# Kernel tuning notes

Measured on AMD Instinct MI355X. Metric: run time of the kernel, lower is better.

## Reference

```python
import math
import jax, jax.numpy as jnp
import numpy as np

B, S, H, I, E = 4, 2048, 1024, 4096, 8
CAPACITY_FACTOR = 1.0


def setup_inputs() -> dict:
    key = jax.random.key(0)
    k1, k2, k3, k4, k5 = jax.random.split(key, 5)
    x = jax.random.normal(k1, (B, S, H), dtype=jnp.float32)
    # Router: nn.Linear(H, E) with xavier_uniform weight, zero-ish bias
    limit = math.sqrt(6.0 / (H + E))
    router_w = jax.random.uniform(k2, (E, H), dtype=jnp.float32, minval=-limit, maxval=limit)
    router_b = jnp.zeros((E,), dtype=jnp.float32)
    # Expert weights (torch.randn init; scaled for numeric sanity)
    experts_inter = jax.random.normal(k3, (E, H, I), dtype=jnp.float32) * 0.02
    experts_out = jax.random.normal(k4, (E, I, H), dtype=jnp.float32) * 0.02
    return {"x": x, "router_w": router_w, "router_b": router_b,
            "experts_inter": experts_inter, "experts_out": experts_out}


def reference(x, router_w, router_b, experts_inter, experts_out):
    b, s, h = x.shape
    e = experts_inter.shape[0]
    capacity = math.ceil(b * s / e * CAPACITY_FACTOR)  # static

    # Router: linear + softmax over experts
    routing_weights = jax.nn.softmax(x @ router_w.T + router_b, axis=-1)  # [b,s,e]

    x_flat = x.reshape(-1, h)                       # [N, h]
    w_flat = routing_weights.reshape(-1, e)         # [N, e]

    # softmax > 0 everywhere, but keep faithful mask-based routing
    routing_mask = (w_flat > 0).astype(jnp.int32)   # [N, e]
    # stable descending sort per expert column (matches stable torch.sort)
    sorted_indices = jnp.argsort(-routing_mask, axis=0, stable=True)  # [N, e]
    sorted_mask = jnp.take_along_axis(routing_mask, sorted_indices, axis=0)[:capacity]  # [c, e]
    sorted_indices = sorted_indices[:capacity]      # [c, e]

    used_tokens_indices = (sorted_indices * sorted_mask).reshape(-1)  # [c*e]
    mask_f = sorted_mask.reshape(-1).astype(x.dtype)[:, None]
    inputs_tokens = x_flat[used_tokens_indices] * mask_f              # [c*e, h]
    inputs_tokens = inputs_tokens.reshape(capacity, e, h)             # [c, e, h]
    inputs_weights = jnp.take_along_axis(w_flat, sorted_indices, axis=0)  # [c, e]

    # grouped expert FFN
    inter = jnp.einsum('ceh,ehi->cei', inputs_tokens, experts_inter)  # [c, e, I]
    inter = jax.nn.relu(inter)
    out = jnp.einsum('cei,eih->ceh', inter, experts_out)              # [c, e, h]
    out = out * inputs_weights[..., None]
    out = out.reshape(-1, h)                                          # [c*e, h]

    # scatter-add combine
    combined = jnp.zeros_like(x_flat).at[used_tokens_indices].add(out)
    return combined.reshape(b, s, h)
```

## Files before the change

### kernel.cpp

```cpp
#include <hip/hip_runtime.h>
#include <stdint.h>

#define H_DIM 1024
#define I_DIM 4096
#define E_NUM 8
#define CAP   1024

typedef __attribute__((ext_vector_type(8))) short bf16x8;
typedef __attribute__((ext_vector_type(4))) float f32x4;

#define AS1 __attribute__((address_space(1)))
#define AS3 __attribute__((address_space(3)))

__device__ __forceinline__ unsigned short f2bf(float f){
  union { float f; uint32_t u; } v; v.f = f;
  uint32_t u = v.u;
  uint32_t r = (u + 0x7FFFu + ((u >> 16) & 1u)) >> 16;
  return (unsigned short)r;
}

__global__ void zero_kernel(float4* __restrict__ p, int n4){
  int i = blockIdx.x*blockDim.x + threadIdx.x;
  int stride = gridDim.x*blockDim.x;
  float4 z; z.x=0.f; z.y=0.f; z.z=0.f; z.w=0.f;
  for (; i < n4; i += stride) p[i] = z;
}

__global__ __launch_bounds__(256) void router_kernel(
    const float* __restrict__ x, const float* __restrict__ rw_w,
    const float* __restrict__ rb, unsigned short* __restrict__ xb,
    float* __restrict__ rwout)
{
  int c = blockIdx.x;
  int t = threadIdx.x;
  float acc[E_NUM];
  #pragma unroll
  for (int e=0;e<E_NUM;e++) acc[e]=0.f;
  const float* xr = x + (size_t)c*H_DIM;
  for (int h=t; h<H_DIM; h+=256){
    float xv = xr[h];
    xb[(size_t)c*H_DIM + h] = f2bf(xv);
    #pragma unroll
    for (int e=0;e<E_NUM;e++) acc[e] += xv * rw_w[e*H_DIM + h];
  }
  __shared__ float part[256][E_NUM];
  #pragma unroll
  for (int e=0;e<E_NUM;e++) part[t][e]=acc[e];
  __syncthreads();
  for (int s=128; s>0; s>>=1){
    if (t<s){
      #pragma unroll
      for (int e=0;e<E_NUM;e++) part[t][e]+=part[t+s][e];
    }
    __syncthreads();
  }
  if (t==0){
    float l[E_NUM], mx=-1e30f;
    #pragma unroll
    for (int e=0;e<E_NUM;e++){ l[e]=part[0][e]+rb[e]; mx=fmaxf(mx,l[e]); }
    float s=0.f;
    #pragma unroll
    for (int e=0;e<E_NUM;e++){ l[e]=expf(l[e]-mx); s+=l[e]; }
    float inv = 1.f/s;
    #pragma unroll
    for (int e=0;e<E_NUM;e++) rwout[c*E_NUM+e] = l[e]*inv;
  }
}

__global__ __launch_bounds__(256) void transpose_cvt(
    const float* __restrict__ src, unsigned short* __restrict__ dst,
    int R, int C, long srcZ, long dstZ)
{
  src += (size_t)blockIdx.z * srcZ;
  dst += (size_t)blockIdx.z * dstZ;
  __shared__ float tile[32][33];
  int c0 = blockIdx.x*32, r0 = blockIdx.y*32;
  int tx = threadIdx.x, ty = threadIdx.y;
  #pragma unroll
  for (int j=ty; j<32; j+=8)
    tile[j][tx] = src[(size_t)(r0+j)*C + c0+tx];
  __syncthreads();
  #pragma unroll
  for (int j=ty; j<32; j+=8)
    dst[(size_t)(c0+j)*R + r0+tx] = f2bf(tile[tx][j]);
}

template<int MODE>
__global__ __launch_bounds__(512, 2) void gemm4b(
    const unsigned short* __restrict__ A, int lda, long aZ,
    const unsigned short* __restrict__ B, int ldb, long bZ,
    int NH, int tilesPerZ,
    const float* __restrict__ rw,
    unsigned short* __restrict__ outInter,
    float* __restrict__ outAdd)
{
  extern __shared__ char smem[];

  int nwg = gridDim.x;
  int id  = blockIdx.x;
  int swz = (id & 7)*(nwg >> 3) + (id >> 3);
  int z   = swz / tilesPerZ;
  int rr_ = swz - z*tilesPerZ;
  int mt  = rr_ & 3, nt = rr_ >> 2;
  int m0  = mt*256, n0 = nt*256;

  const unsigned short* Ab = A + (size_t)z*aZ + (size_t)m0*lda;
  const unsigned short* Bb = B + (size_t)z*bZ + (size_t)n0*ldb;

  int tid  = threadIdx.x;
  int w    = tid >> 6, l = tid & 63;
  int wr   = w >> 2,  wc = w & 3;
  int lrow = l & 15,  lq = l >> 4;

  int rsw = (lq ^ ((lrow>>1)&3)) << 4;

  int srow  = (l >> 2);
  int sslot = ((l & 3) ^ ((l >> 3) & 3)) * 8;
  size_t aOff0 = (size_t)(w*32 + srow)      * lda + sslot;
  size_t aOff1 = (size_t)(w*32 + 16 + srow) * lda + sslot;
  size_t bOff0 = (size_t)(w*32 + srow)      * ldb + sslot;
  size_t bOff1 = (size_t)(w*32 + 16 + srow) * ldb + sslot;
  int ldsA0 = (w*32)*64, ldsA1 = (w*32+16)*64;

  auto stageHalf = [&](int h){
    char* lb = smem + ((h & 3) << 15);
    int kb = h << 5;
    __builtin_amdgcn_global_load_lds((const AS1 void*)(Ab + aOff0 + kb),
        (AS3 void*)(lb + ldsA0), 16, 0, 0);
    __builtin_amdgcn_global_load_lds((const AS1 void*)(Ab + aOff1 + kb),
        (AS3 void*)(lb + ldsA1), 16, 0, 0);
    __builtin_amdgcn_global_load_lds((const AS1 void*)(Bb + bOff0 + kb),
        (AS3 void*)(lb + 16384 + ldsA0), 16, 0, 0);
    __builtin_amdgcn_global_load_lds((const AS1 void*)(Bb + bOff1 + kb),
        (AS3 void*)(lb + 16384 + ldsA1), 16, 0, 0);
  };

  f32x4 acc[8][4];
  #pragma unroll
  for (int i=0;i<8;i++)
    #pragma unroll
    for (int j=0;j<4;j++)
      acc[i][j] = (f32x4){0.f,0.f,0.f,0.f};

  auto compute = [&](int h){
    char* lb = smem + ((h & 3) << 15);
    bf16x8 af[8], bfr[4];
    #pragma unroll
    for (int Mf=0;Mf<8;Mf++)
      af[Mf] = *(const bf16x8*)(lb + (wr*128 + Mf*16 + lrow)*64 + rsw);
    #pragma unroll
    for (int Nf=0;Nf<4;Nf++)
      bfr[Nf] = *(const bf16x8*)(lb + 16384 + (wc*64 + Nf*16 + lrow)*64 + rsw);
    __builtin_amdgcn_s_setprio(1);
    #pragma unroll
    for (int Mf=0;Mf<8;Mf++)
      #pragma unroll
      for (int Nf=0;Nf<4;Nf++)
        acc[Mf][Nf] = __builtin_amdgcn_mfma_f32_16x16x32_bf16(af[Mf], bfr[Nf], acc[Mf][Nf], 0, 0, 0);
    __builtin_amdgcn_s_setprio(0);
  };

  stageHalf(0); stageHalf(1); stageHalf(2);

  int h = 0;
  for (; h < NH-2; ++h){
    asm volatile("s_waitcnt vmcnt(8)" ::: "memory");
    __builtin_amdgcn_s_barrier();
    if (h+3 < NH) stageHalf(h+3);
    compute(h);
  }
  asm volatile("s_waitcnt vmcnt(4)" ::: "memory");
  __builtin_amdgcn_s_barrier();
  compute(NH-2);
  asm volatile("s_waitcnt vmcnt(0)" ::: "memory");
  __builtin_amdgcn_s_barrier();
  compute(NH-1);

  #pragma unroll
  for (int Mf=0;Mf<8;Mf++){
    #pragma unroll
    for (int Nf=0;Nf<4;Nf++){
      #pragma unroll
      for (int rg=0;rg<4;rg++){
        int gm = m0 + wr*128 + Mf*16 + lq*4 + rg;
        int gn = n0 + wc*64 + Nf*16 + lrow;
        float v = acc[Mf][Nf][rg];
        if (MODE==0){
          v = fmaxf(v, 0.f) * rw[gm*E_NUM + z];
          outInter[(size_t)gm*(E_NUM*I_DIM) + (size_t)z*I_DIM + gn] = f2bf(v);
        } else {
          atomicAdd(&outAdd[(size_t)gm*H_DIM + gn], v);
        }
      }
    }
  }
}

extern "C" void kernel_launch(void* const* d_in, const int* in_sizes, int n_in,
                              void* d_out, int out_size, void* d_ws, size_t ws_size,
                              hipStream_t stream)
{
  const float* x   = (const float*)d_in[0];
  const float* rww = (const float*)d_in[1];
  const float* rwb = (const float*)d_in[2];
  const float* w1  = (const float*)d_in[3];
  const float* w2  = (const float*)d_in[4];
  float* out = (float*)d_out;

  char* ws = (char*)d_ws;
  float*          rwout = (float*)(ws);
  unsigned short* xb    = (unsigned short*)(ws + (1u<<16));
  unsigned short* inter = (unsigned short*)(ws + (4ull<<20));
  unsigned short* wt    = (unsigned short*)(ws + (68ull<<20));
  const size_t needed = 132ull<<20;

  zero_kernel<<<2048, 256, 0, stream>>>((float4*)out, out_size/4);
  if (ws_size < needed) return;

  void* k0 = (void*)gemm4b<0>;
  void* k1 = (void*)gemm4b<1>;
  hipFuncSetAttribute(k0, hipFuncAttributeMaxDynamicSharedMemorySize, 131072);
  hipFuncSetAttribute(k1, hipFuncAttributeMaxDynamicSharedMemorySize, 131072);

  router_kernel<<<CAP, 256, 0, stream>>>(x, rww, rwb, xb, rwout);

  dim3 tb(32,8);
  transpose_cvt<<<dim3(I_DIM/32, H_DIM/32, E_NUM), tb, 0, stream>>>(
      w1, wt, H_DIM, I_DIM, (long)H_DIM*I_DIM, (long)I_DIM*H_DIM);

  gemm4b<0><<<512, 512, 131072, stream>>>(
      xb, H_DIM, 0L,
      wt, H_DIM, (long)I_DIM*H_DIM,
      32, 64, rwout, inter, nullptr);

  transpose_cvt<<<dim3(H_DIM/32, (E_NUM*I_DIM)/32, 1), tb, 0, stream>>>(
      w2, wt, E_NUM*I_DIM, H_DIM, 0L, 0L);

  gemm4b<1><<<256, 512, 131072, stream>>>(
      inter, E_NUM*I_DIM, 2048L,
      wt,    E_NUM*I_DIM, 2048L,
      64, 16, nullptr, nullptr, out);
}
```

Baseline: 307.1 us.

## Split GEMM k-step into two phases interleaving A/B prefetch with MFMA halves

Restructures the gemm main loop so each k-step issues the A-tile prefetch, computes the first half of the M fragments, then issues the B-tile prefetch and computes the second half, with explicit lgkmcnt waits, sched barriers and extra workgroup barriers between phases. The goal is to spread global-to-LDS traffic across the iteration and cut register pressure from holding all eight A fragments at once. It adds two extra barriers per k-step and forces full LDS-read drains before the MFMAs, which can stall waves and weaken latency hiding.

```diff
diff --git a/kernel.cpp b/kernel.cpp
--- a/kernel.cpp
+++ b/kernel.cpp
@@ -122,13 +122,17 @@
   size_t bOff1 = (size_t)(w*32 + 16 + srow) * ldb + sslot;
   int ldsA0 = (w*32)*64, ldsA1 = (w*32+16)*64;
 
-  auto stageHalf = [&](int h){
+  auto stageA = [&](int h){
     char* lb = smem + ((h & 3) << 15);
     int kb = h << 5;
     __builtin_amdgcn_global_load_lds((const AS1 void*)(Ab + aOff0 + kb),
         (AS3 void*)(lb + ldsA0), 16, 0, 0);
     __builtin_amdgcn_global_load_lds((const AS1 void*)(Ab + aOff1 + kb),
         (AS3 void*)(lb + ldsA1), 16, 0, 0);
+  };
+  auto stageB = [&](int h){
+    char* lb = smem + ((h & 3) << 15);
+    int kb = h << 5;
     __builtin_amdgcn_global_load_lds((const AS1 void*)(Bb + bOff0 + kb),
         (AS3 void*)(lb + 16384 + ldsA0), 16, 0, 0);
     __builtin_amdgcn_global_load_lds((const AS1 void*)(Bb + bOff1 + kb),
@@ -142,39 +146,53 @@
     for (int j=0;j<4;j++)
       acc[i][j] = (f32x4){0.f,0.f,0.f,0.f};
 
-  auto compute = [&](int h){
+  stageA(0); stageB(0); stageA(1); stageB(1); stageA(2); stageB(2);
+
+  for (int h = 0; h < NH; ++h){
+    int pend = NH-1-h; if (pend > 2) pend = 2;
+    if (pend == 2)      asm volatile("s_waitcnt vmcnt(8)" ::: "memory");
+    else if (pend == 1) asm volatile("s_waitcnt vmcnt(4)" ::: "memory");
+    else                asm volatile("s_waitcnt vmcnt(0)" ::: "memory");
+    __builtin_amdgcn_s_barrier();
+
     char* lb = smem + ((h & 3) << 15);
-    bf16x8 af[8], bfr[4];
-    #pragma unroll
-    for (int Mf=0;Mf<8;Mf++)
-      af[Mf] = *(const bf16x8*)(lb + (wr*128 + Mf*16 + lrow)*64 + rsw);
+    bool pf = (h+3 < NH);
+
+    if (pf) stageA(h+3);
+    bf16x8 af0[4], bfr[4];
+    #pragma unroll
+    for (int Mf=0;Mf<4;Mf++)
+      af0[Mf] = *(const bf16x8*)(lb + (wr*128 + Mf*16 + lrow)*64 + rsw);
     #pragma unroll
     for (int Nf=0;Nf<4;Nf++)
       bfr[Nf] = *(const bf16x8*)(lb + 16384 + (wc*64 + Nf*16 + lrow)*64 + rsw);
+    asm volatile("s_waitcnt lgkmcnt(0)" ::: "memory");
+    __builtin_amdgcn_sched_barrier(0);
     __builtin_amdgcn_s_setprio(1);
     #pragma unroll
-    for (int Mf=0;Mf<8;Mf++)
+    for (int Mf=0;Mf<4;Mf++)
       #pragma unroll
       for (int Nf=0;Nf<4;Nf++)
-        acc[Mf][Nf] = __builtin_amdgcn_mfma_f32_16x16x32_bf16(af[Mf], bfr[Nf], acc[Mf][Nf], 0, 0, 0);
+        acc[Mf][Nf] = __builtin_amdgcn_mfma_f32_16x16x32_bf16(af0[Mf], bfr[Nf], acc[Mf][Nf], 0, 0, 0);
     __builtin_amdgcn_s_setprio(0);
-  };
-
-  stageHalf(0); stageHalf(1); stageHalf(2);
-
-  int h = 0;
-  for (; h < NH-2; ++h){
-    asm volatile("s_waitcnt vmcnt(8)" ::: "memory");
     __builtin_amdgcn_s_barrier();
-    if (h+3 < NH) stageHalf(h+3);
-    compute(h);
-  }
-  asm volatile("s_waitcnt vmcnt(4)" ::: "memory");
-  __builtin_amdgcn_s_barrier();
-  compute(NH-2);
-  asm volatile("s_waitcnt vmcnt(0)" ::: "memory");
-  __builtin_amdgcn_s_barrier();
-  compute(NH-1);
+
+    if (pf) stageB(h+3);
+    bf16x8 af1[4];
+    #pragma unroll
+    for (int Mf=0;Mf<4;Mf++)
+      af1[Mf] = *(const bf16x8*)(lb + (wr*128 + (Mf+4)*16 + lrow)*64 + rsw);
+    asm volatile("s_waitcnt lgkmcnt(0)" ::: "memory");
+    __builtin_amdgcn_sched_barrier(0);
+    __builtin_amdgcn_s_setprio(1);
+    #pragma unroll
+    for (int Mf=0;Mf<4;Mf++)
+      #pragma unroll
+      for (int Nf=0;Nf<4;Nf++)
+        acc[Mf+4][Nf] = __builtin_amdgcn_mfma_f32_16x16x32_bf16(af1[Mf], bfr[Nf], acc[Mf+4][Nf], 0, 0, 0);
+    __builtin_amdgcn_s_setprio(0);
+    __builtin_amdgcn_s_barrier();
+  }
 
   #pragma unroll
   for (int Mf=0;Mf<8;Mf++){
```

After: 311.4 us. Within noise of the previous version (+1.4%).

## Switch GEMM to 32x32x16 MFMA and vectorize weight transpose with 64x64 tiles

Applied to the files above, without the earlier changes.

The GEMM inner loop moves from 16x16x32 bf16 MFMA to 32x32x16 bf16 MFMA with 16-float accumulators. The LDS fragment addressing and the epilogue index mapping are rewritten to match. This halves the number of fragment loads per MFMA and should raise arithmetic intensity per LDS read. Separately, the fp32-to-bf16 weight transpose now uses 64x64 tiles with float4 loads and ushort4 stores to cut memory transaction count. The new lane mappings risk LDS bank conflicts under the existing swizzle.

```diff
diff --git a/kernel.cpp b/kernel.cpp
--- a/kernel.cpp
+++ b/kernel.cpp
@@ -7,7 +7,7 @@
 #define CAP   1024
 
 typedef __attribute__((ext_vector_type(8))) short bf16x8;
-typedef __attribute__((ext_vector_type(4))) float f32x4;
+typedef __attribute__((ext_vector_type(16))) float f32x16;
 
 #define AS1 __attribute__((address_space(1)))
 #define AS3 __attribute__((address_space(3)))
@@ -67,22 +67,33 @@
   }
 }
 
-__global__ __launch_bounds__(256) void transpose_cvt(
+__global__ __launch_bounds__(256) void transpose_cvt64(
     const float* __restrict__ src, unsigned short* __restrict__ dst,
     int R, int C, long srcZ, long dstZ)
 {
   src += (size_t)blockIdx.z * srcZ;
   dst += (size_t)blockIdx.z * dstZ;
-  __shared__ float tile[32][33];
-  int c0 = blockIdx.x*32, r0 = blockIdx.y*32;
-  int tx = threadIdx.x, ty = threadIdx.y;
-  #pragma unroll
-  for (int j=ty; j<32; j+=8)
-    tile[j][tx] = src[(size_t)(r0+j)*C + c0+tx];
+  __shared__ float tile[64][65];
+  int c0 = blockIdx.x*64, r0 = blockIdx.y*64;
+  int t  = threadIdx.x;
+  int tx = t & 15, ty = t >> 4;
+  #pragma unroll
+  for (int p=0;p<4;p++){
+    int r = ty + p*16;
+    float4 v = *(const float4*)(src + (size_t)(r0+r)*C + c0 + tx*4);
+    tile[r][tx*4+0]=v.x; tile[r][tx*4+1]=v.y; tile[r][tx*4+2]=v.z; tile[r][tx*4+3]=v.w;
+  }
   __syncthreads();
   #pragma unroll
-  for (int j=ty; j<32; j+=8)
-    dst[(size_t)(c0+j)*R + r0+tx] = f2bf(tile[tx][j]);
+  for (int p=0;p<4;p++){
+    int c = ty + p*16;
+    ushort4 o;
+    o.x = f2bf(tile[tx*4+0][c]);
+    o.y = f2bf(tile[tx*4+1][c]);
+    o.z = f2bf(tile[tx*4+2][c]);
+    o.w = f2bf(tile[tx*4+3][c]);
+    *(ushort4*)(dst + (size_t)(c0+c)*R + r0 + tx*4) = o;
+  }
 }
 
 template<int MODE>
@@ -110,9 +121,6 @@
   int tid  = threadIdx.x;
   int w    = tid >> 6, l = tid & 63;
   int wr   = w >> 2,  wc = w & 3;
-  int lrow = l & 15,  lq = l >> 4;
-
-  int rsw = (lq ^ ((lrow>>1)&3)) << 4;
 
   int srow  = (l >> 2);
   int sslot = ((l & 3) ^ ((l >> 3) & 3)) * 8;
@@ -135,28 +143,40 @@
         (AS3 void*)(lb + 16384 + ldsA1), 16, 0, 0);
   };
 
-  f32x4 acc[8][4];
-  #pragma unroll
-  for (int i=0;i<8;i++)
-    #pragma unroll
-    for (int j=0;j<4;j++)
-      acc[i][j] = (f32x4){0.f,0.f,0.f,0.f};
+  f32x16 acc[4][2];
+  #pragma unroll
+  for (int i=0;i<4;i++)
+    #pragma unroll
+    for (int j=0;j<2;j++)
+      acc[i][j] = (f32x16){0.f,0.f,0.f,0.f,0.f,0.f,0.f,0.f,
+                           0.f,0.f,0.f,0.f,0.f,0.f,0.f,0.f};
+
+  int arow = wr*128 + (l&31);
+  int brow = wc*64  + (l&31);
+  int ksl  = l >> 5;
+  int sw   = (l >> 1) & 3;
 
   auto compute = [&](int h){
     char* lb = smem + ((h & 3) << 15);
-    bf16x8 af[8], bfr[4];
-    #pragma unroll
-    for (int Mf=0;Mf<8;Mf++)
-      af[Mf] = *(const bf16x8*)(lb + (wr*128 + Mf*16 + lrow)*64 + rsw);
-    #pragma unroll
-    for (int Nf=0;Nf<4;Nf++)
-      bfr[Nf] = *(const bf16x8*)(lb + 16384 + (wc*64 + Nf*16 + lrow)*64 + rsw);
+    bf16x8 af[4][2], bfq[2][2];
+    #pragma unroll
+    for (int fa=0; fa<4; fa++)
+      #pragma unroll
+      for (int kk=0; kk<2; kk++)
+        af[fa][kk] = *(const bf16x8*)(lb + (arow + fa*32)*64 + (((kk*2 + ksl) ^ sw) << 4));
+    #pragma unroll
+    for (int fb=0; fb<2; fb++)
+      #pragma unroll
+      for (int kk=0; kk<2; kk++)
+        bfq[fb][kk] = *(const bf16x8*)(lb + 16384 + (brow + fb*32)*64 + (((kk*2 + ksl) ^ sw) << 4));
     __builtin_amdgcn_s_setprio(1);
     #pragma unroll
-    for (int Mf=0;Mf<8;Mf++)
-      #pragma unroll
-      for (int Nf=0;Nf<4;Nf++)
-        acc[Mf][Nf] = __builtin_amdgcn_mfma_f32_16x16x32_bf16(af[Mf], bfr[Nf], acc[Mf][Nf], 0, 0, 0);
+    for (int kk=0;kk<2;kk++)
+      #pragma unroll
+      for (int fa=0;fa<4;fa++)
+        #pragma unroll
+        for (int fb=0;fb<2;fb++)
+          acc[fa][fb] = __builtin_amdgcn_mfma_f32_32x32x16_bf16(af[fa][kk], bfq[fb][kk], acc[fa][fb], 0, 0, 0);
     __builtin_amdgcn_s_setprio(0);
   };
 
@@ -177,14 +197,14 @@
   compute(NH-1);
 
   #pragma unroll
-  for (int Mf=0;Mf<8;Mf++){
-    #pragma unroll
-    for (int Nf=0;Nf<4;Nf++){
-      #pragma unroll
-      for (int rg=0;rg<4;rg++){
-        int gm = m0 + wr*128 + Mf*16 + lq*4 + rg;
-        int gn = n0 + wc*64 + Nf*16 + lrow;
-        float v = acc[Mf][Nf][rg];
+  for (int fa=0; fa<4; fa++){
+    #pragma unroll
+    for (int fb=0; fb<2; fb++){
+      #pragma unroll
+      for (int rg=0; rg<16; rg++){
+        int gm = m0 + wr*128 + fa*32 + (rg&3) + 8*(rg>>2) + 4*(l>>5);
+        int gn = n0 + wc*64  + fb*32 + (l&31);
+        float v = acc[fa][fb][rg];
         if (MODE==0){
           v = fmaxf(v, 0.f) * rw[gm*E_NUM + z];
           outInter[(size_t)gm*(E_NUM*I_DIM) + (size_t)z*I_DIM + gn] = f2bf(v);
@@ -224,8 +244,7 @@
 
   router_kernel<<<CAP, 256, 0, stream>>>(x, rww, rwb, xb, rwout);
 
-  dim3 tb(32,8);
-  transpose_cvt<<<dim3(I_DIM/32, H_DIM/32, E_NUM), tb, 0, stream>>>(
+  transpose_cvt64<<<dim3(I_DIM/64, H_DIM/64, E_NUM), 256, 0, stream>>>(
       w1, wt, H_DIM, I_DIM, (long)H_DIM*I_DIM, (long)I_DIM*H_DIM);
 
   gemm4b<0><<<512, 512, 131072, stream>>>(
@@ -233,7 +252,7 @@
       wt, H_DIM, (long)I_DIM*H_DIM,
       32, 64, rwout, inter, nullptr);
 
-  transpose_cvt<<<dim3(H_DIM/32, (E_NUM*I_DIM)/32, 1), tb, 0, stream>>>(
+  transpose_cvt64<<<dim3(H_DIM/64, (E_NUM*I_DIM)/64, 1), 256, 0, stream>>>(
       w2, wt, E_NUM*I_DIM, H_DIM, 0L, 0L);
 
   gemm4b<1><<<256, 512, 131072, stream>>>(
```

New measurement: 274.6 us. 10.6% less time.
